# Kernel optimization log

Hardware: AMD Instinct MI355X
Metric: run time of the kernel (lower is better)

Reference implementation:

```python
import jax, jax.numpy as jnp
import numpy as np

N_USER, N_ITEM, N_BUNDLE = 200000, 100000, 50000
EMBED_DIM = 128
B, L = 8192, 100  # batch of bundles, max items per bundle


def setup_inputs() -> dict:
    key = jax.random.key(0)
    ks = jax.random.split(key, 12)
    d, d2 = EMBED_DIM, 2 * EMBED_DIM
    x_u = jax.random.randint(ks[0], (B,), 0, N_USER)
    x_b = jax.random.randint(ks[1], (B,), 0, N_BUNDLE)
    items = jax.random.randint(ks[2], (B, L), 0, N_ITEM)
    # ragged bundle sizes in [10, L]; padded+masked form of the CSR gather
    lengths = jax.random.randint(ks[3], (B,), 10, L + 1)
    mask = jnp.arange(L)[None, :] < lengths[:, None]  # [B, L] bool
    return {
        "x_u": x_u,
        "x_b": x_b,
        "items": items,
        "mask": mask,
        "emb_u": jax.random.normal(ks[4], (N_USER, d), jnp.float32) * 0.1,
        "emb_i": jax.random.normal(ks[5], (N_ITEM, d), jnp.float32) * 0.1,
        "emb_b": jax.random.normal(ks[6], (N_BUNDLE, d), jnp.float32) * 0.1,
        "A": jax.random.normal(ks[7], (N_ITEM, d), jnp.float32) * 0.1,
        "fc1_w": jax.random.normal(ks[8], (d2, d2), jnp.float32) / np.sqrt(d2),
        "fc1_b": jnp.zeros((d2,), jnp.float32),
        "fc2_w": jax.random.normal(ks[9], (d2, d2), jnp.float32) / np.sqrt(d2),
        "fc2_b": jnp.zeros((d2,), jnp.float32),
        "out_w": jax.random.normal(ks[10], (1, d2), jnp.float32) / np.sqrt(d2),
        "out_b": jnp.zeros((1,), jnp.float32),
    }


def reference(x_u, x_b, items, mask, emb_u, emb_i, emb_b, A,
              fc1_w, fc1_b, fc2_w, fc2_b, out_w, out_b):
    # DAM.forward_bundle with the attention() per-bundle loop vectorized
    h_u = emb_u[x_u]                       # [B, d]
    h_b = emb_b[x_b]                       # [B, d]
    item_e = emb_i[items]                  # [B, L, d] ragged gather (padded)
    a_e = A[items]                         # [B, L, d]
    # w = softmax_l( sum_d e_u * A[item] ) per bundle, over valid items only
    scores = jnp.einsum('bd,bld->bl', h_u, a_e)
    scores = jnp.where(mask, scores, -jnp.inf)
    w = jax.nn.softmax(scores, axis=1)     # [B, L]
    h_x = jnp.einsum('bl,bld->bd', w, item_e)
    h = jnp.concatenate([h_u, h_b + h_x], axis=1)   # [B, 2d]
    h = jax.nn.leaky_relu(h @ fc1_w.T + fc1_b)
    h = jax.nn.leaky_relu(h @ fc2_w.T + fc2_b)
    return h @ out_w.T + out_b             # [B, 1]
```

## Files before the change

### kernel.cpp

```cpp
#include <hip/hip_runtime.h>
#include <hip/hip_bf16.h>

#define D   128
#define D2  256
#define H1P 272

typedef short bf16x8 __attribute__((ext_vector_type(8)));
typedef float f32x4  __attribute__((ext_vector_type(4)));

__device__ __forceinline__ float bf2f(unsigned short u) {
    return __uint_as_float(((unsigned int)u) << 16);
}
__device__ __forceinline__ float bflo(unsigned int p) { return __uint_as_float(p << 16); }
__device__ __forceinline__ float bfhi(unsigned int p) { return __uint_as_float(p & 0xffff0000u); }
__device__ __forceinline__ unsigned short f2bf(float f) {
    __hip_bfloat16 h = __float2bfloat16(f);
    return *(unsigned short*)&h;
}

template<bool BF>
__device__ __forceinline__ float ld1(const void* p, size_t i) {
    if constexpr (BF) return bf2f(((const unsigned short*)p)[i]);
    else              return ((const float*)p)[i];
}

template<bool BF>
__device__ __forceinline__ void load8f(const void* p, size_t elem_off, float* r) {
    if constexpr (BF) {
        uint4 v = *(const uint4*)((const unsigned short*)p + elem_off);
        r[0]=bflo(v.x); r[1]=bfhi(v.x); r[2]=bflo(v.y); r[3]=bfhi(v.y);
        r[4]=bflo(v.z); r[5]=bfhi(v.z); r[6]=bflo(v.w); r[7]=bfhi(v.w);
    } else {
        const float4* q = (const float4*)((const float*)p + elem_off);
        float4 a = q[0], b = q[1];
        r[0]=a.x; r[1]=a.y; r[2]=a.z; r[3]=a.w;
        r[4]=b.x; r[5]=b.y; r[6]=b.z; r[7]=b.w;
    }
}

__device__ __forceinline__ void store8bf(unsigned short* p, const float* r) {
    union { unsigned short u[8]; uint4 v; } pk;
    #pragma unroll
    for (int k = 0; k < 8; ++k) pk.u[k] = f2bf(r[k]);
    *(uint4*)p = pk.v;
}

__device__ __forceinline__ bool read_mask(const void* mask, int mmode, size_t i) {
    if (mmode == 0) return ((const int*)mask)[i] != 0;
    if (mmode == 1) return ((const unsigned char*)mask)[i] != 0;
    return ((const unsigned short*)mask)[i] != 0;
}

__device__ __forceinline__ bool probe_is_bf16(const unsigned int* probe) {
    const int lane = threadIdx.x & 63;
    int cnt = 0;
    #pragma unroll
    for (int i = 0; i < 4; ++i) {
        unsigned int e = (probe[lane + 64 * i] >> 7) & 0xffu;
        cnt += (e >= 90 && e < 130) ? 1 : 0;
    }
    #pragma unroll
    for (int o = 32; o; o >>= 1) cnt += __shfl_xor(cnt, o);
    return cnt >= 128;
}

template<bool BF>
__device__ __forceinline__ void attn_wave(
    const int* __restrict__ x_u, const int* __restrict__ x_b,
    const int* __restrict__ items, const void* __restrict__ mask, int mmode,
    const void* __restrict__ emb_u, const void* __restrict__ emb_i,
    const void* __restrict__ emb_b, const void* __restrict__ Aw,
    unsigned short* __restrict__ h_out, int L)
{
    const int lane = threadIdx.x & 63;
    const int wv   = threadIdx.x >> 6;
    const int b    = blockIdx.x * 4 + wv;

    const int xu = x_u[b], xb = x_b[b];

    const int  c0 = (lane < L) ? lane : 0;
    int  i0 = items[(size_t)b * L + c0];
    bool v0 = (lane < L) && read_mask(mask, mmode, (size_t)b * L + c0);
    int  i1 = i0;
    bool v1 = false;
    if (64 + lane < L) {
        i1 = items[(size_t)b * L + 64 + lane];
        v1 = read_mask(mask, mmode, (size_t)b * L + 64 + lane);
    }
    const int len = __popcll(__ballot(v0)) + __popcll(__ballot(v1));

    const int seg = lane & 3;
    float hu[32];
    #pragma unroll
    for (int j = 0; j < 4; ++j)
        load8f<BF>(emb_u, (size_t)xu * D + seg * 32 + j * 8, hu + j * 8);

    const int itm4 = lane >> 2;
    float e[7];
    float e_sum = 0.f;
    #pragma unroll
    for (int c = 0; c < 7; ++c) {
        e[c] = 0.f;
        if (c == 0 || c * 16 < len) {
            const int i  = c * 16 + itm4;
            const int id = (c < 4) ? __shfl(i0, i) : __shfl(i1, i - 64);
            float acc = 0.f, r[8];
            #pragma unroll
            for (int j = 0; j < 4; ++j) {
                load8f<BF>(Aw, (size_t)id * D + seg * 32 + j * 8, r);
                #pragma unroll
                for (int k = 0; k < 8; ++k) acc += hu[j * 8 + k] * r[k];
            }
            acc += __shfl_xor(acc, 1);
            acc += __shfl_xor(acc, 2);
            const float ev = (i < len) ? __expf(acc) : 0.f;
            e[c] = ev;
            if ((lane & 3) == 0) e_sum += ev;
        }
    }
    #pragma unroll
    for (int o = 32; o; o >>= 1) e_sum += __shfl_xor(e_sum, o);
    const float inv = (e_sum > 0.f) ? 1.f / e_sum : 0.f;

    const int g = lane >> 4, m16 = lane & 15;
    float acc8[8];
    #pragma unroll
    for (int k = 0; k < 8; ++k) acc8[k] = 0.f;
    #pragma unroll
    for (int p = 0; p < 13; ++p) {
        if (p == 0 || p * 8 < len) {
            const int ia = p * 8 + g, ib = ia + 4;
            const int ida = (p < 8) ? __shfl(i0, ia) : __shfl(i1, ia - 64);
            const int idb = (p < 8) ? __shfl(i0, ib) : __shfl(i1, ib - 64);
            const float wa = __shfl(e[p >> 1], (ia & 15) << 2);
            const float wb = __shfl(e[p >> 1], (ib & 15) << 2);
            float ra[8], rb[8];
            load8f<BF>(emb_i, (size_t)ida * D + m16 * 8, ra);
            load8f<BF>(emb_i, (size_t)idb * D + m16 * 8, rb);
            #pragma unroll
            for (int k = 0; k < 8; ++k) acc8[k] += wa * ra[k] + wb * rb[k];
        }
    }
    #pragma unroll
    for (int k = 0; k < 8; ++k) {
        acc8[k] += __shfl_xor(acc8[k], 16);
        acc8[k] += __shfl_xor(acc8[k], 32);
    }

    if (g == 0) {
        if constexpr (BF) {
            uint4 raw = *(const uint4*)((const unsigned short*)emb_u
                                        + (size_t)xu * D + m16 * 8);
            *(uint4*)(h_out + (size_t)b * D2 + m16 * 8) = raw;
        } else {
            float r[8];
            load8f<false>(emb_u, (size_t)xu * D + m16 * 8, r);
            store8bf(h_out + (size_t)b * D2 + m16 * 8, r);
        }
        float rb2[8], outv[8];
        load8f<BF>(emb_b, (size_t)xb * D + m16 * 8, rb2);
        #pragma unroll
        for (int k = 0; k < 8; ++k) outv[k] = rb2[k] + acc8[k] * inv;
        store8bf(h_out + (size_t)b * D2 + D + m16 * 8, outv);
    }
}

__global__ __launch_bounds__(256) void attn_kernel(
    const int* x_u, const int* x_b, const int* items, const void* mask,
    const void* emb_u, const void* emb_i, const void* emb_b, const void* A,
    unsigned short* h_out, int L)
{
    const bool bf = probe_is_bf16((const unsigned int*)emb_u);
    const unsigned char* mb = (const unsigned char*)mask;
    const int mm = (mb[1] == 0) ? 0 : ((mb[0] == 1) ? 1 : 2);

    if (bf) attn_wave<true >(x_u, x_b, items, mask, mm, emb_u, emb_i, emb_b, A, h_out, L);
    else    attn_wave<false>(x_u, x_b, items, mask, mm, emb_u, emb_i, emb_b, A, h_out, L);
}

template<bool BF>
__device__ __forceinline__ bf16x8 load_w8(const void* W, size_t off) {
    if constexpr (BF) {
        return *(const bf16x8*)((const unsigned short*)W + off);
    } else {
        const float* p = (const float*)W + off;
        float4 a = *(const float4*)p;
        float4 b = *(const float4*)(p + 4);
        bf16x8 r;
        r[0] = (short)f2bf(a.x); r[1] = (short)f2bf(a.y);
        r[2] = (short)f2bf(a.z); r[3] = (short)f2bf(a.w);
        r[4] = (short)f2bf(b.x); r[5] = (short)f2bf(b.y);
        r[6] = (short)f2bf(b.z); r[7] = (short)f2bf(b.w);
        return r;
    }
}

template<bool BF>
__device__ __forceinline__ void mlp_body(
    const unsigned short* __restrict__ X,
    const void* __restrict__ fc1_w, const void* __restrict__ fc1_b,
    const void* __restrict__ fc2_w, const void* __restrict__ fc2_b,
    const void* __restrict__ out_w, const void* __restrict__ out_b,
    void* __restrict__ out,
    unsigned short* h1_s, float (*po_s)[16])
{
    const int tid  = threadIdx.x;
    const int wave = tid >> 6;
    const int lane = tid & 63;
    const int l16  = lane & 15;
    const int quad = lane >> 4;
    const int mt   = blockIdx.x * 16;

    bf16x8 afrag[8];
    const size_t abase = (size_t)(mt + l16) * D2 + quad * 8;
    #pragma unroll
    for (int kc = 0; kc < 8; ++kc)
        afrag[kc] = *(const bf16x8*)(X + abase + kc * 32);

    #pragma unroll
    for (int jj = 0; jj < 4; ++jj) {
        const int jt = wave * 4 + jj;
        const size_t bbase = (size_t)(jt * 16 + l16) * D2 + quad * 8;
        f32x4 acc = {0.f, 0.f, 0.f, 0.f};
        #pragma unroll
        for (int kc = 0; kc < 8; ++kc) {
            bf16x8 bfrag = load_w8<BF>(fc1_w, bbase + kc * 32);
            acc = __builtin_amdgcn_mfma_f32_16x16x32_bf16(afrag[kc], bfrag, acc, 0, 0, 0);
        }
        const int j  = jt * 16 + l16;
        const float bj = ld1<BF>(fc1_b, j);
        #pragma unroll
        for (int r = 0; r < 4; ++r) {
            float v = acc[r] + bj;
            v = v > 0.f ? v : 0.01f * v;
            h1_s[(quad * 4 + r) * H1P + j] = f2bf(v);
        }
    }
    __syncthreads();

    bf16x8 afrag2[8];
    #pragma unroll
    for (int kc = 0; kc < 8; ++kc)
        afrag2[kc] = *(const bf16x8*)&h1_s[l16 * H1P + quad * 8 + kc * 32];

    float po[4] = {0.f, 0.f, 0.f, 0.f};
    #pragma unroll
    for (int jj = 0; jj < 4; ++jj) {
        const int jt = wave * 4 + jj;
        const size_t bbase = (size_t)(jt * 16 + l16) * D2 + quad * 8;
        f32x4 acc = {0.f, 0.f, 0.f, 0.f};
        #pragma unroll
        for (int kc = 0; kc < 8; ++kc) {
            bf16x8 bfrag = load_w8<BF>(fc2_w, bbase + kc * 32);
            acc = __builtin_amdgcn_mfma_f32_16x16x32_bf16(afrag2[kc], bfrag, acc, 0, 0, 0);
        }
        const int j  = jt * 16 + l16;
        const float bj = ld1<BF>(fc2_b, j);
        const float wj = ld1<BF>(out_w, j);
        #pragma unroll
        for (int r = 0; r < 4; ++r) {
            float v = acc[r] + bj;
            v = v > 0.f ? v : 0.01f * v;
            po[r] += v * wj;
        }
    }
    #pragma unroll
    for (int r = 0; r < 4; ++r) {
        #pragma unroll
        for (int o = 1; o < 16; o <<= 1) po[r] += __shfl_xor(po[r], o);
    }
    if (l16 == 0) {
        #pragma unroll
        for (int r = 0; r < 4; ++r) po_s[wave][quad * 4 + r] = po[r];
    }
    __syncthreads();

    if (tid < 16) {
        const float v = po_s[0][tid] + po_s[1][tid] + po_s[2][tid] + po_s[3][tid]
                      + ld1<BF>(out_b, 0);
        if constexpr (BF) ((unsigned short*)out)[mt + tid] = f2bf(v);
        else              ((float*)out)[mt + tid] = v;
    }
}

__global__ __launch_bounds__(256) void mlp_kernel(
    const unsigned short* X,
    const void* fc1_w, const void* fc1_b, const void* fc2_w, const void* fc2_b,
    const void* out_w, const void* out_b, void* out, const void* probe)
{
    __shared__ unsigned short h1_s[16 * H1P];
    __shared__ float po_s[4][16];

    const bool bf = probe_is_bf16((const unsigned int*)probe);
    if (bf) mlp_body<true >(X, fc1_w, fc1_b, fc2_w, fc2_b, out_w, out_b, out, h1_s, po_s);
    else    mlp_body<false>(X, fc1_w, fc1_b, fc2_w, fc2_b, out_w, out_b, out, h1_s, po_s);
}

extern "C" void kernel_launch(void* const* d_in, const int* in_sizes, int n_in,
                              void* d_out, int out_size, void* d_ws, size_t ws_size,
                              hipStream_t stream) {
    const int*  x_u   = (const int*)d_in[0];
    const int*  x_b   = (const int*)d_in[1];
    const int*  items = (const int*)d_in[2];
    const void* mask  = d_in[3];
    const void* emb_u = d_in[4];
    const void* emb_i = d_in[5];
    const void* emb_b = d_in[6];
    const void* A     = d_in[7];
    const void* fc1_w = d_in[8];
    const void* fc1_b = d_in[9];
    const void* fc2_w = d_in[10];
    const void* fc2_b = d_in[11];
    const void* out_w = d_in[12];
    const void* out_b = d_in[13];

    const int B = in_sizes[0];
    const int L = in_sizes[2] / B;

    unsigned short* h = (unsigned short*)d_ws;

    attn_kernel<<<B / 4, 256, 0, stream>>>(x_u, x_b, items, mask,
                                           emb_u, emb_i, emb_b, A, h, L);
    mlp_kernel<<<B / 16, 256, 0, stream>>>(h, fc1_w, fc1_b, fc2_w, fc2_b,
                                           out_w, out_b, d_out, emb_u);
}
```

Measured before the change: 313.8 us.

## Fuse attention score and weighted item sum into one software-pipelined pass

Merges the two phases (computing scores from A rows, then weighted-summing emb_i rows) into a single loop where each 16-lane group handles one item, loading its A row and emb_i row together. Scores are reduced across 16 lanes, exponentiated and applied immediately, which removes the cross-lane weight redistribution and the separate e[] buffer. Loads are prefetched up to three iterations ahead to hide gather latency. The loop now has a runtime trip count instead of a fully unrolled one, and the deeper reduction uses more shuffles per item.

```diff
diff --git a/kernel.cpp b/kernel.cpp
--- a/kernel.cpp
+++ b/kernel.cpp
@@ -38,6 +38,11 @@
     }
 }
 
+__device__ __forceinline__ void unpack8(uint4 v, float* r) {
+    r[0]=bflo(v.x); r[1]=bfhi(v.x); r[2]=bflo(v.y); r[3]=bfhi(v.y);
+    r[4]=bflo(v.z); r[5]=bfhi(v.z); r[6]=bflo(v.w); r[7]=bfhi(v.w);
+}
+
 __device__ __forceinline__ void store8bf(unsigned short* p, const float* r) {
     union { unsigned short u[8]; uint4 v; } pk;
     #pragma unroll
@@ -89,63 +94,92 @@
     }
     const int len = __popcll(__ballot(v0)) + __popcll(__ballot(v1));
 
-    const int seg = lane & 3;
-    float hu[32];
-    #pragma unroll
-    for (int j = 0; j < 4; ++j)
-        load8f<BF>(emb_u, (size_t)xu * D + seg * 32 + j * 8, hu + j * 8);
-
-    const int itm4 = lane >> 2;
-    float e[7];
-    float e_sum = 0.f;
-    #pragma unroll
-    for (int c = 0; c < 7; ++c) {
-        e[c] = 0.f;
-        if (c == 0 || c * 16 < len) {
-            const int i  = c * 16 + itm4;
-            const int id = (c < 4) ? __shfl(i0, i) : __shfl(i1, i - 64);
-            float acc = 0.f, r[8];
-            #pragma unroll
-            for (int j = 0; j < 4; ++j) {
-                load8f<BF>(Aw, (size_t)id * D + seg * 32 + j * 8, r);
-                #pragma unroll
-                for (int k = 0; k < 8; ++k) acc += hu[j * 8 + k] * r[k];
-            }
-            acc += __shfl_xor(acc, 1);
-            acc += __shfl_xor(acc, 2);
-            const float ev = (i < len) ? __expf(acc) : 0.f;
-            e[c] = ev;
-            if ((lane & 3) == 0) e_sum += ev;
-        }
-    }
-    #pragma unroll
-    for (int o = 32; o; o >>= 1) e_sum += __shfl_xor(e_sum, o);
-    const float inv = (e_sum > 0.f) ? 1.f / e_sum : 0.f;
-
     const int g = lane >> 4, m16 = lane & 15;
+
+    float hu8[8];
+    load8f<BF>(emb_u, (size_t)xu * D + m16 * 8, hu8);
+
+    const int NP = (len + 3) >> 2;
+
+    auto get_id = [&](int p) -> int {
+        const int idx = 4 * p + g;
+        const int src = (idx < len) ? idx : 0;
+        return (src < 64) ? __shfl(i0, src) : __shfl(i1, src - 64);
+    };
+
+    float esum = 0.f;
     float acc8[8];
     #pragma unroll
     for (int k = 0; k < 8; ++k) acc8[k] = 0.f;
-    #pragma unroll
-    for (int p = 0; p < 13; ++p) {
-        if (p == 0 || p * 8 < len) {
-            const int ia = p * 8 + g, ib = ia + 4;
-            const int ida = (p < 8) ? __shfl(i0, ia) : __shfl(i1, ia - 64);
-            const int idb = (p < 8) ? __shfl(i0, ib) : __shfl(i1, ib - 64);
-            const float wa = __shfl(e[p >> 1], (ia & 15) << 2);
-            const float wb = __shfl(e[p >> 1], (ib & 15) << 2);
-            float ra[8], rb[8];
-            load8f<BF>(emb_i, (size_t)ida * D + m16 * 8, ra);
-            load8f<BF>(emb_i, (size_t)idb * D + m16 * 8, rb);
-            #pragma unroll
-            for (int k = 0; k < 8; ++k) acc8[k] += wa * ra[k] + wb * rb[k];
-        }
-    }
+
+    if constexpr (BF) {
+        const unsigned short* AW = (const unsigned short*)Aw;
+        const unsigned short* EI = (const unsigned short*)emb_i;
+        auto fetch = [&](int p, uint4& a, uint4& v) {
+            const int id = get_id(p);
+            a = *(const uint4*)(AW + (size_t)id * D + m16 * 8);
+            v = *(const uint4*)(EI + (size_t)id * D + m16 * 8);
+        };
+        uint4 a0, u0, a1, u1, a2, u2;
+        fetch(0, a0, u0);
+        fetch(1, a1, u1);
+        if (2 < NP) fetch(2, a2, u2);
+        for (int p = 0; p < NP; ++p) {
+            const uint4 ca = a0, cv = u0;
+            a0 = a1; u0 = u1; a1 = a2; u1 = u2;
+            if (p + 3 < NP) fetch(p + 3, a2, u2);
+            float af[8];
+            unpack8(ca, af);
+            float s = 0.f;
+            #pragma unroll
+            for (int k = 0; k < 8; ++k) s += hu8[k] * af[k];
+            s += __shfl_xor(s, 1); s += __shfl_xor(s, 2);
+            s += __shfl_xor(s, 4); s += __shfl_xor(s, 8);
+            const int idx = 4 * p + g;
+            const float e = (idx < len) ? __expf(s) : 0.f;
+            esum += e;
+            float vf[8];
+            unpack8(cv, vf);
+            #pragma unroll
+            for (int k = 0; k < 8; ++k) acc8[k] += e * vf[k];
+        }
+    } else {
+        auto fetchf = [&](int p, float* a, float* v) {
+            const int id = get_id(p);
+            load8f<false>(Aw,    (size_t)id * D + m16 * 8, a);
+            load8f<false>(emb_i, (size_t)id * D + m16 * 8, v);
+        };
+        float a0[8], u0[8], a1[8], u1[8];
+        fetchf(0, a0, u0);
+        if (1 < NP) fetchf(1, a1, u1);
+        for (int p = 0; p < NP; ++p) {
+            float ca[8], cv[8];
+            #pragma unroll
+            for (int k = 0; k < 8; ++k) { ca[k] = a0[k]; cv[k] = u0[k]; }
+            #pragma unroll
+            for (int k = 0; k < 8; ++k) { a0[k] = a1[k]; u0[k] = u1[k]; }
+            if (p + 2 < NP) fetchf(p + 2, a1, u1);
+            float s = 0.f;
+            #pragma unroll
+            for (int k = 0; k < 8; ++k) s += hu8[k] * ca[k];
+            s += __shfl_xor(s, 1); s += __shfl_xor(s, 2);
+            s += __shfl_xor(s, 4); s += __shfl_xor(s, 8);
+            const int idx = 4 * p + g;
+            const float e = (idx < len) ? __expf(s) : 0.f;
+            esum += e;
+            #pragma unroll
+            for (int k = 0; k < 8; ++k) acc8[k] += e * cv[k];
+        }
+    }
+
+    esum += __shfl_xor(esum, 16);
+    esum += __shfl_xor(esum, 32);
     #pragma unroll
     for (int k = 0; k < 8; ++k) {
         acc8[k] += __shfl_xor(acc8[k], 16);
         acc8[k] += __shfl_xor(acc8[k], 32);
     }
+    const float inv = (esum > 0.f) ? 1.f / esum : 0.f;
 
     if (g == 0) {
         if constexpr (BF) {
```

After: 305.5 us. 1.03x faster.
